# Optimization experiments

Measured on AMD Instinct MI355X. Metric: run time of the kernel, lower is better.

## Reference

```python
import jax, jax.numpy as jnp
import numpy as np

N, C, E, NUM_ID, NUM_LABELS = 50000, 128, 1600000, 2048, 7


def setup_inputs() -> dict:
    key = jax.random.key(0)
    k_x, k_r, k_c, k_id, k_lab, k_w, k_wid = jax.random.split(key, 7)
    x = jax.random.normal(k_x, (N, C), dtype=jnp.float32)
    row = jax.random.randint(k_r, (E,), 0, N)
    col = jax.random.randint(k_c, (E,), 0, N)
    # remove accidental self-loops so the 'add remaining self loops' step
    # (append all N self loops) matches PyG's add_remaining_self_loops exactly
    col = jnp.where(col == row, (col + 1) % N, col)
    edge_index = jnp.stack([row, col]).astype(jnp.int64)
    idx = jax.random.randint(k_id, (NUM_ID,), 0, N).astype(jnp.int64)
    node_label = jax.random.randint(k_lab, (N,), 0, 8).astype(jnp.int64)
    # glorot init
    s = jnp.sqrt(6.0 / (C + C)).astype(jnp.float32)
    weight = jax.random.uniform(k_w, (C, C), minval=-s, maxval=s, dtype=jnp.float32)
    weight_id = jax.random.uniform(k_wid, (NUM_LABELS, C, C), minval=-s, maxval=s, dtype=jnp.float32)
    return {"x": x, "edge_index": edge_index, "id": idx, "node_label": node_label,
            "weight": weight, "weight_id": weight_id}


def reference(x, edge_index, id, node_label, weight, weight_id):
    n = x.shape[0]
    row, col = edge_index[0], edge_index[1]
    # ego-center update: x[id] += x[id] @ W (index_add handles duplicate ids)
    x = x.at[id].add(x[id] @ weight)
    # label-grouped gather-matmul-scatter: ox = x + sum_i mask_i * (x @ W_i)
    ox = x
    for i in range(NUM_LABELS):
        mask = (node_label == i + 1)
        ox = ox + jnp.where(mask[:, None], x @ weight_id[i], jnp.zeros((), x.dtype))
    # GCN symmetric normalization with self loops (fill_value = 1.0)
    loop = jnp.arange(n)
    row_f = jnp.concatenate([row, loop])
    col_f = jnp.concatenate([col, loop])
    ew = jnp.ones((row_f.shape[0],), dtype=x.dtype)
    deg = jax.ops.segment_sum(ew, row_f, num_segments=n)
    dinv = jnp.where(deg > 0, deg ** -0.5, jnp.zeros((), x.dtype))
    norm = dinv[row_f] * ew * dinv[col_f]
    # message = norm * x_j (source row), aggregated by sum at target col
    out = jax.ops.segment_sum(norm[:, None] * ox[row_f], col_f, num_segments=n)
    return out
```

## Files before the change

kernel.cpp:

```cpp
#include <hip/hip_runtime.h>
#include <hip/hip_bf16.h>

typedef unsigned int   u32;
typedef unsigned short u16;
typedef unsigned char  u8;
typedef float f32x2 __attribute__((ext_vector_type(2)));
typedef float f32x4 __attribute__((ext_vector_type(4)));

#define N_NODES 50000
#define C_DIM   128
#define E_EDGES 1600000
#define NUM_IDX 2048

#define CPB 256
#define NB  196
#define CAP 9216
#define CHK 8192
#define NP  196
#define PT  512
#define EPT 16
#define GB  8
#define NLB 98


__global__ void part_hist_kernel(const int* __restrict__ row, const int* __restrict__ col,
                                 const int* __restrict__ label, const int* __restrict__ id,
                                 int* __restrict__ colCursor, int* __restrict__ rowCursor,
                                 u32* __restrict__ S, u8* __restrict__ Sr,
                                 int* __restrict__ labCnt, int* __restrict__ cnt) {
    __shared__ int hc[NB], hr[NB], bc[NB], br[NB];
    __shared__ int h8[8];
    int t = threadIdx.x;
    if (blockIdx.x >= NP) {
        if (t < 8) h8[t] = 0;
        __syncthreads();
        int n = (blockIdx.x - NP) * PT + t;
        if (n < N_NODES) atomicAdd(&h8[label[n]], 1);
        if (n < NUM_IDX) atomicAdd(&cnt[id[n]], 1);
        __syncthreads();
        if (t < 8 && h8[t] > 0) atomicAdd(&labCnt[t], h8[t]);
        return;
    }
    int p = blockIdx.x;
    for (int i = t; i < NB; i += PT) { hc[i] = 0; hr[i] = 0; }
    __syncthreads();
    int e0 = p * CHK, e1 = min(e0 + CHK, E_EDGES);
    int rr[EPT], cc[EPT];
    #pragma unroll
    for (int i = 0; i < EPT; ++i) {
        int e = e0 + t + i * PT;
        if (e < e1) {
            int r = row[e], c = col[e];
            rr[i] = r; cc[i] = c;
            atomicAdd(&hc[c >> 8], 1);
            atomicAdd(&hr[r >> 8], 1);
        }
    }
    __syncthreads();
    for (int i = t; i < NB; i += PT) {
        bc[i] = (hc[i] > 0) ? (i * CAP + atomicAdd(&colCursor[i], hc[i])) : 0;
        br[i] = (hr[i] > 0) ? (i * CAP + atomicAdd(&rowCursor[i], hr[i])) : 0;
    }
    __syncthreads();
    #pragma unroll
    for (int i = 0; i < EPT; ++i) {
        int e = e0 + t + i * PT;
        if (e < e1) {
            int r = rr[i], c = cc[i];
            int pc = atomicAdd(&bc[c >> 8], 1);
            S[pc] = ((u32)r << 8) | (u32)(c & 255);
            int pr = atomicAdd(&br[r >> 8], 1);
            Sr[pr] = (u8)(r & 255);
        }
    }
}

__global__ void csr_fill_kernel(const u32* __restrict__ S, const u8* __restrict__ Sr,
                                const int* __restrict__ colCursor, const int* __restrict__ rowCursor,
                                int* __restrict__ s_beg, int* __restrict__ s_end,
                                u16* __restrict__ srcrow, float* __restrict__ dinv,
                                const int* __restrict__ label, const int* __restrict__ labCnt,
                                int* __restrict__ labOffset, int* __restrict__ nodeByLabel) {
    __shared__ int h[CPB], cur[CPB], sc[CPB];
    __shared__ int h8[8], base8[8], c28[8];
    int t = threadIdx.x;
    if (blockIdx.x >= 2 * NB) {
        if (t < 8) { h8[t] = 0; c28[t] = 0; }
        __syncthreads();
        int n = (blockIdx.x - 2 * NB) * PT + t;
        int l = 0;
        if (n < N_NODES) { l = label[n]; atomicAdd(&h8[l], 1); }
        __syncthreads();
        if (t < 8 && h8[t] > 0) {
            int lb = 0;
            for (int i = 0; i < t; ++i) lb += labCnt[i];
            base8[t] = lb + atomicAdd(&labOffset[t], h8[t]);
        }
        __syncthreads();
        if (n < N_NODES) {
            int pos = base8[l] + atomicAdd(&c28[l], 1);
            nodeByLabel[pos] = n;
        }
        return;
    }
    if (blockIdx.x >= NB) {
        int b = blockIdx.x - NB;
        if (t < CPB) h[t] = 0;
        __syncthreads();
        int e0 = b * CAP, e1 = b * CAP + rowCursor[b];
        for (int e = e0 + t; e < e1; e += PT) atomicAdd(&h[Sr[e]], 1);
        __syncthreads();
        if (t < CPB) {
            int n = b * CPB + t;
            if (n < N_NODES) dinv[n] = rsqrtf((float)(h[t] + 1));
        }
        return;
    }
    int b = blockIdx.x;
    if (t < CPB) h[t] = 0;
    __syncthreads();
    int e0 = b * CAP, e1 = b * CAP + colCursor[b];
    for (int e = e0 + t; e < e1; e += PT) atomicAdd(&h[S[e] & 255u], 1);
    __syncthreads();
    if (t < CPB) sc[t] = h[t];
    __syncthreads();
    for (int off = 1; off < CPB; off <<= 1) {
        int v = 0, a = 0;
        if (t < CPB) { v = sc[t]; a = (t >= off) ? sc[t - off] : 0; }
        __syncthreads();
        if (t < CPB) sc[t] = v + a;
        __syncthreads();
    }
    if (t < CPB) {
        int base = (t == 0) ? 0 : sc[t - 1];
        int gcol = b * CPB + t;
        if (gcol < N_NODES) {
            s_beg[gcol] = e0 + base;
            s_end[gcol] = e0 + base + h[t];
        }
        cur[t] = base;
    }
    __syncthreads();
    for (int e = e0 + t; e < e1; e += PT) {
        u32 v = S[e];
        int pos = atomicAdd(&cur[v & 255u], 1);
        srcrow[e0 + pos] = (u16)(v >> 8);
    }
}

__global__ void node_msg_kernel(const float* __restrict__ x,
                                const int* __restrict__ cnt,
                                const int* __restrict__ label,
                                const float* __restrict__ dinv,
                                const float* __restrict__ W,
                                const float* __restrict__ Wid,
                                const int* __restrict__ nodeByLabel,
                                __hip_bfloat16* __restrict__ msgb) {
    __shared__ float xsT[C_DIM][GB];
    __shared__ int nid[GB], lab[GB], cc[GB];
    int t = threadIdx.x;
    if (t < GB) {
        int n = nodeByLabel[blockIdx.x * GB + t];
        nid[t] = n; lab[t] = label[n]; cc[t] = cnt[n];
    }
    __syncthreads();
    #pragma unroll
    for (int g = 0; g < GB; ++g)
        xsT[t][g] = __builtin_nontemporal_load(x + (size_t)nid[g] * C_DIM + t);
    __syncthreads();
    for (int g = 0; g < GB; ++g) {
        int c = cc[g];
        if (c > 0) {
            float acc = 0.f;
            #pragma unroll 8
            for (int k = 0; k < C_DIM; ++k) acc += xsT[k][g] * W[k * C_DIM + t];
            __syncthreads();
            xsT[t][g] += (float)c * acc;
            __syncthreads();
        }
    }
    float res[GB];
    #pragma unroll
    for (int g = 0; g < GB; ++g) res[g] = xsT[t][g];
    if (lab[0] == lab[GB - 1]) {
        int L = lab[0];
        if (L > 0) {
            const float* Wl = Wid + (size_t)(L - 1) * C_DIM * C_DIM;
            float acc[GB];
            #pragma unroll
            for (int g = 0; g < GB; ++g) acc[g] = 0.f;
            for (int k = 0; k < C_DIM; ++k) {
                float w = Wl[k * C_DIM + t];
                f32x4 xv0 = *(const f32x4*)&xsT[k][0];
                f32x4 xv1 = *(const f32x4*)&xsT[k][4];
                acc[0] += xv0.x * w; acc[1] += xv0.y * w;
                acc[2] += xv0.z * w; acc[3] += xv0.w * w;
                acc[4] += xv1.x * w; acc[5] += xv1.y * w;
                acc[6] += xv1.z * w; acc[7] += xv1.w * w;
            }
            #pragma unroll
            for (int g = 0; g < GB; ++g) res[g] += acc[g];
        }
    } else {
        for (int g = 0; g < GB; ++g) {
            int L = lab[g];
            if (L > 0) {
                const float* Wl = Wid + (size_t)(L - 1) * C_DIM * C_DIM;
                float acc = 0.f;
                #pragma unroll 8
                for (int k = 0; k < C_DIM; ++k) acc += xsT[k][g] * Wl[k * C_DIM + t];
                res[g] += acc;
            }
        }
    }
    #pragma unroll
    for (int g = 0; g < GB; ++g) {
        int n = nid[g];
        msgb[(size_t)n * C_DIM + t] = __float2bfloat16(dinv[n] * res[g]);
    }
}

__global__ void gather_kernel(const int* __restrict__ s_beg, const int* __restrict__ s_end,
                              const u16* __restrict__ srcrow,
                              const float* __restrict__ dinv,
                              const u32* __restrict__ m32,
                              float* __restrict__ out) {
    int wid  = threadIdx.x >> 6;
    int lane = threadIdx.x & 63;
    int g = lane >> 4;
    int q = lane & 15;
    int c = blockIdx.x * 4 + wid;
    int e0 = s_beg[c], e1 = s_end[c];
    const uint4* m4 = (const uint4*)m32;

    float a0[4], a1[4];
    #pragma unroll
    for (int k = 0; k < 4; ++k) { a0[k] = 0.f; a1[k] = 0.f; }

    #define ACC4(U)                                                          \
        a0[0] += __uint_as_float((U).x << 16); a1[0] += __uint_as_float((U).x & 0xffff0000u); \
        a0[1] += __uint_as_float((U).y << 16); a1[1] += __uint_as_float((U).y & 0xffff0000u); \
        a0[2] += __uint_as_float((U).z << 16); a1[2] += __uint_as_float((U).z & 0xffff0000u); \
        a0[3] += __uint_as_float((U).w << 16); a1[3] += __uint_as_float((U).w & 0xffff0000u);

    int e = e0;
    for (; e + 8 <= e1; e += 8) {
        u32 r0 = srcrow[e + g];
        u32 r1 = srcrow[e + 4 + g];
        uint4 u0 = m4[r0 * 16u + (u32)q];
        uint4 u1 = m4[r1 * 16u + (u32)q];
        ACC4(u0);
        ACC4(u1);
    }
    if (e + 4 <= e1) {
        u32 r0 = srcrow[e + g];
        uint4 u0 = m4[r0 * 16u + (u32)q];
        ACC4(u0);
        e += 4;
    }
    if (g == 0) {
        uint4 us = m4[(u32)c * 16u + (u32)q];
        ACC4(us);
        for (; e < e1; ++e) {
            u32 r = srcrow[e];
            uint4 u = m4[r * 16u + (u32)q];
            ACC4(u);
        }
    }
    #undef ACC4

    #pragma unroll
    for (int k = 0; k < 4; ++k) {
        a0[k] += __shfl_xor(a0[k], 16);
        a0[k] += __shfl_xor(a0[k], 32);
        a1[k] += __shfl_xor(a1[k], 16);
        a1[k] += __shfl_xor(a1[k], 32);
    }

    if (lane < 16) {
        float di = dinv[c];
        f32x4 o0, o1;
        o0.x = di * a0[0]; o0.y = di * a1[0]; o0.z = di * a0[1]; o0.w = di * a1[1];
        o1.x = di * a0[2]; o1.y = di * a1[2]; o1.z = di * a0[3]; o1.w = di * a1[3];
        f32x4* op = (f32x4*)(out + ((size_t)c << 7)) + (q << 1);
        __builtin_nontemporal_store(o0, op);
        __builtin_nontemporal_store(o1, op + 1);
    }
}

extern "C" void kernel_launch(void* const* d_in, const int* in_sizes, int n_in,
                              void* d_out, int out_size, void* d_ws, size_t ws_size,
                              hipStream_t stream) {
    const float* x     = (const float*)d_in[0];
    const int*   edge  = (const int*)d_in[1];
    const int*   id    = (const int*)d_in[2];
    const int*   label = (const int*)d_in[3];
    const float* W     = (const float*)d_in[4];
    const float* Wid   = (const float*)d_in[5];
    float*       out   = (float*)d_out;

    const int* row = edge;
    const int* col = edge + E_EDGES;

    __hip_bfloat16* msgb = (__hip_bfloat16*)d_ws;
    u32* S           = (u32*)(msgb + (size_t)N_NODES * C_DIM);
    u16* srcrow      = (u16*)(S + (size_t)NB * CAP);
    u8*  Sr          = (u8*)(srcrow + (size_t)NB * CAP);
    int* s_beg       = (int*)(Sr + (size_t)NB * CAP);
    int* s_end       = s_beg + N_NODES;
    int* nodeByLabel = s_end + N_NODES;
    float* dinv      = (float*)(nodeByLabel + N_NODES);
    int* cnt         = (int*)(dinv + N_NODES);
    int* labCnt      = cnt + N_NODES;
    int* labOffset   = labCnt + 8;
    int* colCursor   = labOffset + 8;
    int* rowCursor   = colCursor + NB;

    hipMemsetAsync(cnt, 0, ((size_t)N_NODES + 16 + 2 * NB) * sizeof(int), stream);

    part_hist_kernel<<<NP + NLB, PT, 0, stream>>>(row, col, label, id,
                                                  colCursor, rowCursor, S, Sr, labCnt, cnt);
    csr_fill_kernel <<<2 * NB + NLB, PT, 0, stream>>>(S, Sr, colCursor, rowCursor,
                                                      s_beg, s_end, srcrow, dinv,
                                                      label, labCnt, labOffset, nodeByLabel);
    node_msg_kernel <<<N_NODES / GB, C_DIM, 0, stream>>>(x, cnt, label, dinv, W, Wid,
                                                         nodeByLabel, msgb);
    gather_kernel   <<<N_NODES / 4, 256, 0, stream>>>(s_beg, s_end, srcrow, dinv,
                                                      (const u32*)msgb, out);
}
```

Baseline: 220.5 us.

## Split bf16 message gather into four channel-slice passes for cache locality

Result: slower. 272.1 us (+23.4%).

```diff
diff --git a/kernel.cpp b/kernel.cpp
--- a/kernel.cpp
+++ b/kernel.cpp
@@ -220,18 +220,19 @@
     }
 }
 
-__global__ void gather_kernel(const int* __restrict__ s_beg, const int* __restrict__ s_end,
-                              const u16* __restrict__ srcrow,
-                              const float* __restrict__ dinv,
-                              const u32* __restrict__ m32,
-                              float* __restrict__ out) {
+__global__ void gather_pass_kernel(const int* __restrict__ s_beg, const int* __restrict__ s_end,
+                                   const u16* __restrict__ srcrow,
+                                   const float* __restrict__ dinv,
+                                   const u32* __restrict__ m32,
+                                   float* __restrict__ out, int pass) {
     int wid  = threadIdx.x >> 6;
     int lane = threadIdx.x & 63;
-    int g = lane >> 4;
-    int q = lane & 15;
+    int g = lane >> 2;
+    int q = lane & 3;
     int c = blockIdx.x * 4 + wid;
     int e0 = s_beg[c], e1 = s_end[c];
     const uint4* m4 = (const uint4*)m32;
+    const u32 pq = (u32)(pass * 4 + q);
 
     float a0[4], a1[4];
     #pragma unroll
@@ -243,46 +244,49 @@
         a0[2] += __uint_as_float((U).z << 16); a1[2] += __uint_as_float((U).z & 0xffff0000u); \
         a0[3] += __uint_as_float((U).w << 16); a1[3] += __uint_as_float((U).w & 0xffff0000u);
 
+    if (g == 0) {
+        uint4 us = m4[(u32)c * 16u + pq];
+        ACC4(us);
+    }
     int e = e0;
-    for (; e + 8 <= e1; e += 8) {
-        u32 r0 = srcrow[e + g];
-        u32 r1 = srcrow[e + 4 + g];
-        uint4 u0 = m4[r0 * 16u + (u32)q];
-        uint4 u1 = m4[r1 * 16u + (u32)q];
+    for (; e + 32 <= e1; e += 32) {
+        u32 r0 = __builtin_nontemporal_load(srcrow + e + g);
+        u32 r1 = __builtin_nontemporal_load(srcrow + e + 16 + g);
+        uint4 u0 = m4[r0 * 16u + pq];
+        uint4 u1 = m4[r1 * 16u + pq];
         ACC4(u0);
         ACC4(u1);
     }
-    if (e + 4 <= e1) {
+    for (; e + 16 <= e1; e += 16) {
+        u32 r0 = __builtin_nontemporal_load(srcrow + e + g);
+        uint4 u0 = m4[r0 * 16u + pq];
+        ACC4(u0);
+    }
+    if (e + g < e1) {
         u32 r0 = srcrow[e + g];
-        uint4 u0 = m4[r0 * 16u + (u32)q];
+        uint4 u0 = m4[r0 * 16u + pq];
         ACC4(u0);
-        e += 4;
-    }
-    if (g == 0) {
-        uint4 us = m4[(u32)c * 16u + (u32)q];
-        ACC4(us);
-        for (; e < e1; ++e) {
-            u32 r = srcrow[e];
-            uint4 u = m4[r * 16u + (u32)q];
-            ACC4(u);
-        }
     }
     #undef ACC4
 
     #pragma unroll
     for (int k = 0; k < 4; ++k) {
+        a0[k] += __shfl_xor(a0[k], 4);
+        a0[k] += __shfl_xor(a0[k], 8);
         a0[k] += __shfl_xor(a0[k], 16);
         a0[k] += __shfl_xor(a0[k], 32);
+        a1[k] += __shfl_xor(a1[k], 4);
+        a1[k] += __shfl_xor(a1[k], 8);
         a1[k] += __shfl_xor(a1[k], 16);
         a1[k] += __shfl_xor(a1[k], 32);
     }
 
-    if (lane < 16) {
+    if (lane < 4) {
         float di = dinv[c];
         f32x4 o0, o1;
         o0.x = di * a0[0]; o0.y = di * a1[0]; o0.z = di * a0[1]; o0.w = di * a1[1];
         o1.x = di * a0[2]; o1.y = di * a1[2]; o1.z = di * a0[3]; o1.w = di * a1[3];
-        f32x4* op = (f32x4*)(out + ((size_t)c << 7)) + (q << 1);
+        f32x4* op = (f32x4*)(out + ((size_t)c << 7)) + (pass << 3) + (q << 1);
         __builtin_nontemporal_store(o0, op);
         __builtin_nontemporal_store(o1, op + 1);
     }
@@ -325,6 +329,7 @@
                                                       label, labCnt, labOffset, nodeByLabel);
     node_msg_kernel <<<N_NODES / GB, C_DIM, 0, stream>>>(x, cnt, label, dinv, W, Wid,
                                                          nodeByLabel, msgb);
-    gather_kernel   <<<N_NODES / 4, 256, 0, stream>>>(s_beg, s_end, srcrow, dinv,
-                                                      (const u32*)msgb, out);
-}
+    for (int pass = 0; pass < 4; ++pass)
+        gather_pass_kernel<<<N_NODES / 4, 256, 0, stream>>>(s_beg, s_end, srcrow, dinv,
+                                                            (const u32*)msgb, out, pass);
+}
```
